# Kernel tuning notes

Hardware: AMD Instinct MI355X
Metric: run time of the kernel (lower is better)

The kernel has to match this reference:

```python
import jax, jax.numpy as jnp
import numpy as np
from jax import lax

EPS = 1e-5
HEADS = 4
NPOINT = 512


def _layernorm(x, g, b):
    mu = jnp.mean(x, axis=-1, keepdims=True)
    var = jnp.var(x, axis=-1, keepdims=True)
    return (x - mu) * lax.rsqrt(var + EPS) * g + b


def farthest_point_sample(xyz, npoint):
    # xyz: [B, N, 3] -> idx [B, npoint]  (canonical PointNet++ FPS, seeded at point 0)
    B, N, _ = xyz.shape

    def step(carry, _):
        dist, far = carry  # [B,N], [B]
        centroid = jnp.take_along_axis(xyz, far[:, None, None], axis=1)  # [B,1,3]
        d = jnp.sum((xyz - centroid) ** 2, axis=-1)  # [B,N]
        dist = jnp.minimum(dist, d)
        nxt = jnp.argmax(dist, axis=1).astype(jnp.int32)
        return (dist, nxt), far

    init = (jnp.full((B, N), 1e10, xyz.dtype), jnp.zeros((B,), jnp.int32))
    _, idx = lax.scan(step, init, None, length=npoint)  # [npoint, B]
    return idx.T  # [B, npoint]


def index_points(points, idx):
    # points: [B, N, D], idx: [B, S] -> [B, S, D]
    return jnp.take_along_axis(points, idx[..., None], axis=1)


def setup_inputs() -> dict:
    key = jax.random.key(0)
    ks = iter(jax.random.split(key, 16))
    B, N, Cin, D, Dff, Dout = 8, 2048, 64, 128, 512, 256
    w = lambda k, s: (jax.random.normal(k, s, jnp.float32) * 0.02)
    inp = {
        "xyz": jax.random.normal(next(ks), (B, 3, N), jnp.float32),
        "points": jax.random.normal(next(ks), (B, Cin, N), jnp.float32),
        "W_proj": w(next(ks), (D, Cin)), "b_proj": jnp.zeros((D,)),
        "bn1_g": jnp.ones((D,)), "bn1_b": jnp.zeros((D,)),
        "bn1_m": jnp.zeros((D,)), "bn1_v": jnp.ones((D,)),
        "W_pos": w(next(ks), (D, 3)), "b_pos": jnp.zeros((D,)),
        "Wq": w(next(ks), (D, D)), "bq": jnp.zeros((D,)),
        "Wk": w(next(ks), (D, D)), "bk": jnp.zeros((D,)),
        "Wv": w(next(ks), (D, D)), "bv": jnp.zeros((D,)),
        "Wo": w(next(ks), (D, D)), "bo": jnp.zeros((D,)),
        "ln1_g": jnp.ones((D,)), "ln1_b": jnp.zeros((D,)),
        "W1": w(next(ks), (Dff, D)), "b1": jnp.zeros((Dff,)),
        "W2": w(next(ks), (D, Dff)), "b2": jnp.zeros((D,)),
        "ln2_g": jnp.ones((D,)), "ln2_b": jnp.zeros((D,)),
        "W_fc": w(next(ks), (Dout, D + 3)), "b_fc": jnp.zeros((Dout,)),
        "bn2_g": jnp.ones((Dout,)), "bn2_b": jnp.zeros((Dout,)),
        "bn2_m": jnp.zeros((Dout,)), "bn2_v": jnp.ones((Dout,)),
    }
    return inp


def reference(xyz, points, W_proj, b_proj, bn1_g, bn1_b, bn1_m, bn1_v,
              W_pos, b_pos, Wq, bq, Wk, bk, Wv, bv, Wo, bo,
              ln1_g, ln1_b, W1, b1, W2, b2, ln2_g, ln2_b,
              W_fc, b_fc, bn2_g, bn2_b, bn2_m, bn2_v):
    B, _, N = xyz.shape
    D = W_proj.shape[0]
    hd = D // HEADS

    # project: pointwise conv + BN (inference), output [B, N, D]
    feat = jnp.einsum('dc,bcn->bnd', W_proj, points) + b_proj
    feat = (feat - bn1_m) * lax.rsqrt(bn1_v + EPS) * bn1_g + bn1_b

    # transformer block with xyz positional encoding
    pos = jnp.einsum('dc,bcn->bnd', W_pos, xyz) + b_pos
    x = feat + pos
    q = (x @ Wq.T + bq).reshape(B, N, HEADS, hd)
    k = (x @ Wk.T + bk).reshape(B, N, HEADS, hd)
    v = (x @ Wv.T + bv).reshape(B, N, HEADS, hd)
    scores = jnp.einsum('bnhd,bmhd->bhnm', q, k) / jnp.sqrt(jnp.float32(hd))
    attn = jax.nn.softmax(scores, axis=-1)
    o = jnp.einsum('bhnm,bmhd->bnhd', attn, v).reshape(B, N, D)
    x = _layernorm(x + (o @ Wo.T + bo), ln1_g, ln1_b)
    ffn = jax.nn.relu(x @ W1.T + b1) @ W2.T + b2
    features = _layernorm(x + ffn, ln2_g, ln2_b)  # [B, N, D]

    # sampling + gather
    xyz_t = jnp.transpose(xyz, (0, 2, 1))  # [B, N, 3]
    fps_idx = farthest_point_sample(xyz_t, NPOINT)  # [B, npoint]
    new_points = index_points(features, fps_idx)    # [B, npoint, D]
    new_xyz = index_points(xyz_t, fps_idx)          # [B, npoint, 3]

    cat = jnp.concatenate([new_points, new_xyz], axis=-1)  # [B, npoint, D+3]
    out = jnp.einsum('od,bnd->bon', W_fc, cat) + b_fc[None, :, None]
    out = (out - bn2_m[None, :, None]) * lax.rsqrt(bn2_v + EPS)[None, :, None] \
          * bn2_g[None, :, None] + bn2_b[None, :, None]
    out = jax.nn.relu(out)  # [B, Dout, npoint]

    return jnp.transpose(new_xyz, (0, 2, 1)), out
```

## Files before the change

### kernel.cpp

```cpp
#include <hip/hip_runtime.h>
#include <hip/hip_bf16.h>

#define B_    8
#define N_    2048
#define CIN_  64
#define D_    128
#define DFF_  512
#define DOUT_ 256
#define S_    512
#define H_    4
#define HD_   32
#define EPS_  1e-5f

typedef unsigned short u16;
typedef unsigned long long u64;
typedef __attribute__((ext_vector_type(8))) short short8v;
typedef __attribute__((ext_vector_type(4))) float f32x4;

__device__ __forceinline__ u16 f2bu(float f) {
  __hip_bfloat16 h = __float2bfloat16(f);
  return *(u16*)&h;
}
__device__ __forceinline__ float bu2f(u16 u) {
  __hip_bfloat16 h = *(__hip_bfloat16*)&u;
  return __bfloat162float(h);
}

#define OW_QKV 0
#define OW_O   49152
#define OW_1   65536
#define OW_2   131072
#define OW_FC  196608
#define OW_CAT 237568
#define NW_TOT 249856

__global__ __launch_bounds__(256) void prep_kernel(
    const float* __restrict__ Wq, const float* __restrict__ bq,
    const float* __restrict__ Wk, const float* __restrict__ bk,
    const float* __restrict__ Wv, const float* __restrict__ bv,
    const float* __restrict__ Wo, const float* __restrict__ W1,
    const float* __restrict__ W2, const float* __restrict__ Wfc,
    const float* __restrict__ bfc, const float* __restrict__ Wp,
    const float* __restrict__ bp, const float* __restrict__ Wpos,
    const float* __restrict__ bpos, const float* __restrict__ g1,
    const float* __restrict__ be1, const float* __restrict__ m1,
    const float* __restrict__ v1, const float* __restrict__ g2,
    const float* __restrict__ bb2, const float* __restrict__ m2,
    const float* __restrict__ v2, u16* __restrict__ wb,
    float* __restrict__ fb) {
  const float SC = 0.1767766952966369f;
  int i = blockIdx.x * 256 + threadIdx.x;
  if (i < OW_O) {
    int n = i >> 7, k = i & 127;
    float v = (n < 128) ? Wq[i] * SC
                        : (n < 256) ? Wk[(n - 128) * 128 + k]
                                    : Wv[(n - 256) * 128 + k];
    wb[OW_QKV + i] = f2bu(v);
  } else if (i < OW_1) {
    wb[i] = f2bu(Wo[i - OW_O]);
  } else if (i < OW_2) {
    wb[i] = f2bu(W1[i - OW_1]);
  } else if (i < OW_FC) {
    wb[i] = f2bu(W2[i - OW_2]);
  } else if (i < OW_CAT) {
    int j = i - OW_FC;
    int n = j / 160, c = j % 160;
    wb[i] = f2bu(c < 131 ? Wfc[n * 131 + c] : 0.f);
  } else if (i < NW_TOT) {
    int j = i - OW_CAT;
    int d = j / 96, c = j % 96;
    float v;
    if (c < 64) v = Wp[d * 64 + c] * (g1[d] * rsqrtf(v1[d] + EPS_));
    else if (c < 67) v = Wpos[d * 3 + (c - 64)];
    else v = 0.f;
    wb[i] = f2bu(v);
  } else if (i < NW_TOT + 384) {
    int n = i - NW_TOT;
    fb[n] = (n < 128) ? bq[n] * SC : (n < 256) ? bk[n - 128] : bv[n - 256];
  } else if (i < NW_TOT + 512) {
    int d = i - (NW_TOT + 384);
    float s1 = g1[d] * rsqrtf(v1[d] + EPS_);
    fb[384 + d] = (bp[d] - m1[d]) * s1 + be1[d] + bpos[d];
  } else if (i < NW_TOT + 768) {
    int n = i - (NW_TOT + 512);
    fb[512 + n] = g2[n] * rsqrtf(v2[n] + EPS_);
  } else if (i < NW_TOT + 1024) {
    int n = i - (NW_TOT + 768);
    float s = g2[n] * rsqrtf(v2[n] + EPS_);
    fb[768 + n] = bfc[n] * s + bb2[n] - m2[n] * s;
  }
}

#define FPS_SMEM 256

template <int CTRL, int RM>
__device__ __forceinline__ float dppmax(float v) {
  int m = __builtin_amdgcn_update_dpp(__float_as_int(v), __float_as_int(v),
                                      CTRL, RM, 0xF, true);
  return fmaxf(v, __int_as_float(m));
}

__device__ __forceinline__ void fps_slice(
    char* smem, int b, const float* __restrict__ xyz,
    float* __restrict__ dist_ws, int* __restrict__ far_ws,
    int* __restrict__ idx_out, float* __restrict__ out0, int s0, int s1) {
  u64* keys = (u64*)smem;
  float* crd = (float*)(smem + 64);
  const int t = threadIdx.x, w = t >> 6, lane = t & 63;
  const float* xb = xyz + (size_t)b * 3 * N_;
  const int base = w * 512 + lane * 8;
  float* dw = dist_ws + b * N_;
  float px[8], py[8], pz[8], dist[8];
#pragma unroll
  for (int j = 0; j < 8; j++) {
    px[j] = xb[base + j];
    py[j] = xb[N_ + base + j];
    pz[j] = xb[2 * N_ + base + j];
    dist[j] = 1e10f;
  }
  if (s0 != 0) {
#pragma unroll
    for (int j = 0; j < 8; j++) dist[j] = dw[base + j];
  }
  int far = (s0 == 0) ? 0 : far_ws[b];
  float cx = xb[far], cy = xb[N_ + far], cz = xb[2 * N_ + far];
  for (int s = s0; s < s1; s++) {
    if (t == 0) {
      idx_out[b * S_ + s] = far;
      out0[(size_t)b * 3 * S_ + s] = cx;
      out0[(size_t)b * 3 * S_ + S_ + s] = cy;
      out0[(size_t)b * 3 * S_ + 2 * S_ + s] = cz;
    }
    float best = -1.0f, bx = 0.f, by = 0.f, bz = 0.f;
    int bestp = 0;
#pragma unroll
    for (int j = 0; j < 8; j++) {
      float dx = __fsub_rn(px[j], cx);
      float dy = __fsub_rn(py[j], cy);
      float dz = __fsub_rn(pz[j], cz);
      float d = __fadd_rn(__fadd_rn(__fmul_rn(dx, dx), __fmul_rn(dy, dy)),
                          __fmul_rn(dz, dz));
      float nd = fminf(dist[j], d);
      dist[j] = nd;
      if (nd > best) {
        best = nd; bestp = base + j;
        bx = px[j]; by = py[j]; bz = pz[j];
      }
    }
    float m = best;
    m = dppmax<0x111, 0xF>(m);
    m = dppmax<0x112, 0xF>(m);
    m = dppmax<0x114, 0xF>(m);
    m = dppmax<0x118, 0xF>(m);
    m = dppmax<0x142, 0xA>(m);
    m = dppmax<0x143, 0xC>(m);
    float M = __int_as_float(__builtin_amdgcn_readlane(__float_as_int(m), 63));
    u64 mask = __ballot(best == M);
    int wl = __ffsll((long long)mask) - 1;
    if (lane == wl) {
      int sb = (s & 1) * 4 + w;
      keys[sb] = ((u64)__float_as_uint(M) << 32) |
                 (unsigned)(0xFFFFFFFFu - (unsigned)bestp);
      crd[sb * 3 + 0] = bx;
      crd[sb * 3 + 1] = by;
      crd[sb * 3 + 2] = bz;
    }
    asm volatile("s_waitcnt lgkmcnt(0)" ::: "memory");
    __builtin_amdgcn_s_barrier();
    asm volatile("" ::: "memory");
    const int q0 = (s & 1) * 4;
    u64 k0 = keys[q0], k1 = keys[q0 + 1], k2 = keys[q0 + 2], k3 = keys[q0 + 3];
    float x0 = crd[q0 * 3 + 0], y0 = crd[q0 * 3 + 1], z0 = crd[q0 * 3 + 2];
    float x1 = crd[q0 * 3 + 3], y1 = crd[q0 * 3 + 4], z1 = crd[q0 * 3 + 5];
    float x2 = crd[q0 * 3 + 6], y2 = crd[q0 * 3 + 7], z2 = crd[q0 * 3 + 8];
    float x3 = crd[q0 * 3 + 9], y3 = crd[q0 * 3 + 10], z3 = crd[q0 * 3 + 11];
    bool c01 = k0 >= k1;
    u64 ka = c01 ? k0 : k1;
    float xa = c01 ? x0 : x1, ya = c01 ? y0 : y1, za = c01 ? z0 : z1;
    bool c23 = k2 >= k3;
    u64 kb = c23 ? k2 : k3;
    float xv = c23 ? x2 : x3, yv = c23 ? y2 : y3, zv = c23 ? z2 : z3;
    bool cf = ka >= kb;
    u64 kk = cf ? ka : kb;
    cx = cf ? xa : xv; cy = cf ? ya : yv; cz = cf ? za : zv;
    far = (int)(0xFFFFFFFFu - (unsigned)kk);
  }
#pragma unroll
  for (int j = 0; j < 8; j++) dw[base + j] = dist[j];
  if (t == 0) far_ws[b] = far;
}

template <int K, int KC, int ASTAGE, int EPI>
__global__ __launch_bounds__(256) void gemm_k(
    const u16* __restrict__ A, const u16* __restrict__ W,
    const float* __restrict__ srcf0, const float* __restrict__ srcf1,
    const int* __restrict__ fidx, const float* __restrict__ p0,
    const float* __restrict__ p1, const float* __restrict__ p2,
    const u16* __restrict__ resid, u16* __restrict__ outb,
    float* __restrict__ outf, int ntn, int fpsnb, int s0, int s1,
    const float* fxyz, float* fdist, int* ffar, int* fidxo, float* fout0) {
  constexpr int KP = KC + 8;
  constexpr int GEMM_SMEM = 2 * 128 * KP * 2;
  constexpr int SMEM = GEMM_SMEM > FPS_SMEM ? GEMM_SMEM : FPS_SMEM;
  __shared__ __align__(16) char smem[SMEM];
  if ((int)blockIdx.x < fpsnb) {
    fps_slice(smem, blockIdx.x, fxyz, fdist, ffar, fidxo, fout0, s0, s1);
    return;
  }
  u16 (*As)[KP] = (u16 (*)[KP])smem;
  u16 (*Ws)[KP] = (u16 (*)[KP])(smem + 128 * KP * 2);
  const int bid = blockIdx.x - fpsnb;
  const int mt = bid / ntn, nt = bid % ntn;
  const int t = threadIdx.x, w = t >> 6, lane = t & 63;
  const int g = lane >> 4, lr = lane & 15;

  f32x4 acc[2][8];
#pragma unroll
  for (int qf = 0; qf < 2; qf++)
#pragma unroll
    for (int nf = 0; nf < 8; nf++) acc[qf][nf] = {0.f, 0.f, 0.f, 0.f};

  for (int kc = 0; kc < K / KC; kc++) {
    __syncthreads();
    for (int i = t; i < 128 * (KC / 8); i += 256) {
      int row = i / (KC / 8), c8 = i % (KC / 8);
      *(short8v*)&Ws[row][c8 * 8] =
          *(const short8v*)(W + (size_t)(nt * 128 + row) * K + kc * KC + c8 * 8);
    }
    if constexpr (ASTAGE == 0) {
      for (int i = t; i < 128 * (KC / 8); i += 256) {
        int row = i / (KC / 8), c8 = i % (KC / 8);
        *(short8v*)&As[row][c8 * 8] =
            *(const short8v*)(A + (size_t)(mt * 128 + row) * K + kc * KC + c8 * 8);
      }
    } else if constexpr (ASTAGE == 1) {
      int bb = (mt * 128) >> 11, n0 = (mt * 128) & (N_ - 1);
      for (int i = t; i < 96 * 128; i += 256) {
        int c = i >> 7, n = i & 127;
        float v;
        if (c < 64) v = srcf0[((size_t)bb * CIN_ + c) * N_ + n0 + n];
        else if (c < 67) v = srcf1[((size_t)bb * 3 + (c - 64)) * N_ + n0 + n];
        else v = 0.f;
        As[n][c] = f2bu(v);
      }
    } else {
      int bb = (mt * 128) >> 9, sq0 = (mt * 128) & (S_ - 1);
      for (int i = t; i < 128 * 20; i += 256) {
        int row = i / 20, c8 = i % 20;
        int id = fidx[bb * S_ + sq0 + row];
        short8v val;
        if (c8 < 16) {
          val = *(const short8v*)(A + ((size_t)bb * N_ + id) * D_ + c8 * 8);
        } else if (c8 == 16) {
          val = short8v{0, 0, 0, 0, 0, 0, 0, 0};
          val[0] = (short)f2bu(srcf1[((size_t)bb * 3 + 0) * N_ + id]);
          val[1] = (short)f2bu(srcf1[((size_t)bb * 3 + 1) * N_ + id]);
          val[2] = (short)f2bu(srcf1[((size_t)bb * 3 + 2) * N_ + id]);
        } else {
          val = short8v{0, 0, 0, 0, 0, 0, 0, 0};
        }
        *(short8v*)&As[row][c8 * 8] = val;
      }
    }
    __syncthreads();
#pragma unroll
    for (int ks = 0; ks < KC / 32; ks++) {
      short8v a0 = *(const short8v*)&As[w * 32 + lr][ks * 32 + 8 * g];
      short8v a1 = *(const short8v*)&As[w * 32 + 16 + lr][ks * 32 + 8 * g];
#pragma unroll
      for (int nf = 0; nf < 8; nf++) {
        short8v bb = *(const short8v*)&Ws[nf * 16 + lr][ks * 32 + 8 * g];
        acc[0][nf] = __builtin_amdgcn_mfma_f32_16x16x32_bf16(a0, bb, acc[0][nf], 0, 0, 0);
        acc[1][nf] = __builtin_amdgcn_mfma_f32_16x16x32_bf16(a1, bb, acc[1][nf], 0, 0, 0);
      }
    }
  }

  if constexpr (EPI == 3) {
#pragma unroll
    for (int qf = 0; qf < 2; qf++) {
#pragma unroll
      for (int i = 0; i < 4; i++) {
        int m = mt * 128 + w * 32 + qf * 16 + 4 * g + i;
        float v[8], sm = 0.f, sq = 0.f;
#pragma unroll
        for (int nf = 0; nf < 8; nf++) {
          int n = nf * 16 + lr;
          float x = acc[qf][nf][i] + p0[n] + bu2f(resid[(size_t)m * D_ + n]);
          v[nf] = x;
          sm += x;
          sq += x * x;
        }
#pragma unroll
        for (int msk = 1; msk < 16; msk <<= 1) {
          sm += __shfl_xor(sm, msk);
          sq += __shfl_xor(sq, msk);
        }
        float mu = sm * (1.f / 128.f);
        float var = sq * (1.f / 128.f) - mu * mu;
        float rs = rsqrtf(var + EPS_);
#pragma unroll
        for (int nf = 0; nf < 8; nf++) {
          int n = nf * 16 + lr;
          outb[(size_t)m * D_ + n] = f2bu((v[nf] - mu) * rs * p1[n] + p2[n]);
        }
      }
    }
  } else {
#pragma unroll
    for (int qf = 0; qf < 2; qf++)
#pragma unroll
      for (int nf = 0; nf < 8; nf++)
#pragma unroll
        for (int i = 0; i < 4; i++) {
          int m = mt * 128 + w * 32 + qf * 16 + 4 * g + i;
          int nl = nf * 16 + lr;
          int n = nt * 128 + nl;
          float vv = acc[qf][nf][i];
          if constexpr (EPI == 0) {
            outb[(size_t)m * D_ + nl] = f2bu(vv + p0[n]);
          } else if constexpr (EPI == 1) {
            vv += p0[n];
            int which = n >> 7, h = (n >> 5) & 3, c = n & 31;
            int bb = m >> 11, tok = m & (N_ - 1);
            outb[(size_t)which * 2097152 +
                 (((size_t)bb * H_ + h) * N_ + tok) * HD_ + c] = f2bu(vv);
          } else if constexpr (EPI == 2) {
            outb[(size_t)m * DFF_ + n] = f2bu(fmaxf(vv + p0[n], 0.f));
          } else {
            float r = fmaxf(vv * p1[n] + p2[n], 0.f);
            outf[((size_t)(m >> 9) * DOUT_ + n) * S_ + (m & (S_ - 1))] = r;
          }
        }
  }
}

__global__ __launch_bounds__(256) void attn_mfma_kernel(
    const u16* __restrict__ qg, const u16* __restrict__ kg,
    const u16* __restrict__ vg, u16* __restrict__ o, int fpsnb, int s0, int s1,
    const float* fxyz, float* fdist, int* ffar, int* fidxo, float* fout0) {
  constexpr int ATTN_SMEM = 64 * 40 * 2 + 32 * 72 * 2 + 4 * 16 * 72 * 2;
  constexpr int SMEM = ATTN_SMEM > FPS_SMEM ? ATTN_SMEM : FPS_SMEM;
  __shared__ __align__(16) char smem[SMEM];
  if ((int)blockIdx.x < fpsnb) {
    fps_slice(smem, blockIdx.x, fxyz, fdist, ffar, fidxo, fout0, s0, s1);
    return;
  }
  const int t = threadIdx.x;
  const int w = t >> 6, lane = t & 63, g = lane >> 4, lr = lane & 15;
  u16 (*ks)[40] = (u16 (*)[40])smem;
  u16 (*vt)[72] = (u16 (*)[72])(smem + 5120);
  u16 (*psw)[72] = (u16 (*)[72])(smem + 9728) + w * 16;

  const int bid = blockIdx.x - fpsnb;
  const int qt = bid & 31;
  const int bh = bid >> 5;
  const int b = bh >> 2, h = bh & 3;
  const int qrow = qt * 64 + w * 16 + lr;

  short8v aq = *(const short8v*)(qg + ((size_t)bh * N_ + qrow) * HD_ + 8 * g);

  const u16* kb = kg + (size_t)bh * N_ * HD_;
  const u16* vb = vg + (size_t)bh * N_ * HD_;

  const f32x4 fzero = {0.f, 0.f, 0.f, 0.f};
  float mrun = -INFINITY, lrun = 0.f;
  f32x4 acco[2] = {fzero, fzero};

  const int srow = t >> 2, scol = (t & 3) * 8;

  for (int ch = 0; ch < 32; ch++) {
    __syncthreads();
    short8v kvv = *(const short8v*)(kb + (size_t)(ch * 64 + srow) * HD_ + scol);
    short8v vvv = *(const short8v*)(vb + (size_t)(ch * 64 + srow) * HD_ + scol);
    *(short8v*)(&ks[srow][scol]) = kvv;
#pragma unroll
    for (int e = 0; e < 8; e++) vt[scol + e][srow] = (u16)vvv[e];
    __syncthreads();

    f32x4 st[4];
#pragma unroll
    for (int kt = 0; kt < 4; kt++) {
      short8v ak = *(const short8v*)(&ks[kt * 16 + lr][8 * g]);
      st[kt] = __builtin_amdgcn_mfma_f32_16x16x32_bf16(ak, aq, fzero, 0, 0, 0);
    }

    float mx = -INFINITY;
#pragma unroll
    for (int kt = 0; kt < 4; kt++)
#pragma unroll
      for (int i = 0; i < 4; i++) mx = fmaxf(mx, st[kt][i]);
    mx = fmaxf(mx, __shfl_xor(mx, 16));
    mx = fmaxf(mx, __shfl_xor(mx, 32));
    float nm = fmaxf(mrun, mx);
    float alpha = __expf(mrun - nm);
    mrun = nm;
    float psum = 0.f;
#pragma unroll
    for (int kt = 0; kt < 4; kt++) {
      float p0 = __expf(st[kt][0] - nm);
      float p1 = __expf(st[kt][1] - nm);
      float p2 = __expf(st[kt][2] - nm);
      float p3 = __expf(st[kt][3] - nm);
      psum += (p0 + p1) + (p2 + p3);
      u64 pk = (u64)f2bu(p0) | ((u64)f2bu(p1) << 16) |
               ((u64)f2bu(p2) << 32) | ((u64)f2bu(p3) << 48);
      *(u64*)(&psw[lr][kt * 16 + 4 * g]) = pk;
    }
    psum += __shfl_xor(psum, 16);
    psum += __shfl_xor(psum, 32);
    lrun = lrun * alpha + psum;
#pragma unroll
    for (int dt = 0; dt < 2; dt++)
#pragma unroll
      for (int i = 0; i < 4; i++) acco[dt][i] *= alpha;

#pragma unroll
    for (int mc = 0; mc < 2; mc++) {
      short8v pb = *(const short8v*)(&psw[lr][mc * 32 + 8 * g]);
#pragma unroll
      for (int dt = 0; dt < 2; dt++) {
        short8v av = *(const short8v*)(&vt[dt * 16 + lr][mc * 32 + 8 * g]);
        acco[dt] = __builtin_amdgcn_mfma_f32_16x16x32_bf16(av, pb, acco[dt], 0, 0, 0);
      }
    }
  }

  float rl = 1.0f / lrun;
#pragma unroll
  for (int dt = 0; dt < 2; dt++) {
    u64 pk = (u64)f2bu(acco[dt][0] * rl) | ((u64)f2bu(acco[dt][1] * rl) << 16) |
             ((u64)f2bu(acco[dt][2] * rl) << 32) |
             ((u64)f2bu(acco[dt][3] * rl) << 48);
    *(u64*)(o + ((size_t)b * N_ + qrow) * D_ + h * HD_ + dt * 16 + 4 * g) = pk;
  }
}

extern "C" void kernel_launch(void* const* d_in, const int* in_sizes, int n_in,
                              void* d_out, int out_size, void* d_ws, size_t ws_size,
                              hipStream_t stream) {
  const float* xyz    = (const float*)d_in[0];
  const float* points = (const float*)d_in[1];
  const float* Wp     = (const float*)d_in[2];
  const float* bp     = (const float*)d_in[3];
  const float* g1     = (const float*)d_in[4];
  const float* be1    = (const float*)d_in[5];
  const float* m1     = (const float*)d_in[6];
  const float* v1     = (const float*)d_in[7];
  const float* Wpos   = (const float*)d_in[8];
  const float* bpos   = (const float*)d_in[9];
  const float* Wq     = (const float*)d_in[10];
  const float* bq     = (const float*)d_in[11];
  const float* Wk     = (const float*)d_in[12];
  const float* bk     = (const float*)d_in[13];
  const float* Wv     = (const float*)d_in[14];
  const float* bv     = (const float*)d_in[15];
  const float* Wo     = (const float*)d_in[16];
  const float* bo     = (const float*)d_in[17];
  const float* lg1    = (const float*)d_in[18];
  const float* lb1    = (const float*)d_in[19];
  const float* W1     = (const float*)d_in[20];
  const float* b1     = (const float*)d_in[21];
  const float* W2     = (const float*)d_in[22];
  const float* b2p    = (const float*)d_in[23];
  const float* lg2    = (const float*)d_in[24];
  const float* lb2    = (const float*)d_in[25];
  const float* Wfc    = (const float*)d_in[26];
  const float* bfc    = (const float*)d_in[27];
  const float* g2     = (const float*)d_in[28];
  const float* bb2    = (const float*)d_in[29];
  const float* m2     = (const float*)d_in[30];
  const float* v2     = (const float*)d_in[31];

  float* out0 = (float*)d_out;
  float* out1 = out0 + (size_t)B_ * 3 * S_;

  char* ws = (char*)d_ws;
  int*   fps_idx = (int*)ws;
  u16*   wb      = (u16*)(ws + 16384);
  float* fb      = (float*)(ws + 516096);
  float* dist_ws = (float*)(ws + 520192);
  int*   far_ws  = (int*)(ws + 585728);
  const size_t MB = 1024 * 1024;
  u16* x     = (u16*)(ws + 1 * MB);
  u16* o     = (u16*)(ws + 5 * MB);
  u16* x2    = (u16*)(ws + 9 * MB);
  u16* feats = (u16*)(ws + 13 * MB);
  u16* qb    = (u16*)(ws + 17 * MB);
  u16* h     = (u16*)(ws + 29 * MB);

  prep_kernel<<<980, 256, 0, stream>>>(Wq, bq, Wk, bk, Wv, bv, Wo, W1, W2, Wfc,
                                       bfc, Wp, bp, Wpos, bpos, g1, be1, m1, v1,
                                       g2, bb2, m2, v2, wb, fb);

  gemm_k<96, 96, 1, 0><<<8 + 128, 256, 0, stream>>>(
      nullptr, wb + OW_CAT, points, xyz, nullptr, fb + 384, nullptr, nullptr,
      nullptr, x, nullptr, 1, 8, 0, 70, xyz, dist_ws, far_ws, fps_idx, out0);
  gemm_k<128, 128, 0, 1><<<8 + 384, 256, 0, stream>>>(
      x, wb + OW_QKV, nullptr, nullptr, nullptr, fb, nullptr, nullptr,
      nullptr, qb, nullptr, 3, 8, 70, 160, xyz, dist_ws, far_ws, fps_idx, out0);
  attn_mfma_kernel<<<8 + B_ * H_ * (N_ / 64), 256, 0, stream>>>(
      qb, qb + 2097152, qb + 2 * 2097152, o, 8, 160, 260, xyz, dist_ws, far_ws,
      fps_idx, out0);
  gemm_k<128, 128, 0, 3><<<8 + 128, 256, 0, stream>>>(
      o, wb + OW_O, nullptr, nullptr, nullptr, bo, lg1, lb1, x, x2, nullptr, 1,
      8, 260, 330, xyz, dist_ws, far_ws, fps_idx, out0);
  gemm_k<128, 128, 0, 2><<<8 + 512, 256, 0, stream>>>(
      x2, wb + OW_1, nullptr, nullptr, nullptr, b1, nullptr, nullptr,
      nullptr, h, nullptr, 4, 8, 330, 440, xyz, dist_ws, far_ws, fps_idx, out0);
  gemm_k<512, 128, 0, 3><<<8 + 128, 256, 0, stream>>>(
      h, wb + OW_2, nullptr, nullptr, nullptr, b2p, lg2, lb2, x2, feats,
      nullptr, 1, 8, 440, 512, xyz, dist_ws, far_ws, fps_idx, out0);
  gemm_k<160, 160, 2, 4><<<64, 256, 0, stream>>>(
      feats, wb + OW_FC, nullptr, xyz, fps_idx, nullptr, fb + 512, fb + 768,
      nullptr, nullptr, out1, 2, 0, 0, 0, nullptr, nullptr, nullptr, nullptr,
      nullptr);
}
```

Measured before the change: 360.6 us.

## Widen attention blocks to 512 threads, swizzle LDS, rebalance FPS slices

The attention kernel moves to 512-thread blocks covering 128 query rows, with K and V staging split between the two thread halves. The transposed V and P tiles get XOR-style swizzled LDS layouts to avoid bank conflicts. The softmax now uses exp2 with log2(e) folded into the Q scale. FPS is templated on the wave count so the co-scheduled FPS blocks in attention run 8 waves with 4 points per lane at raised priority, and the FPS step ranges per kernel are shifted to give attention a larger share. The aim is to shorten the serial FPS critical path hidden behind the GEMMs and to speed up attention, at the cost of more LDS per block and possibly lower occupancy.

```diff
diff --git a/kernel.cpp b/kernel.cpp
--- a/kernel.cpp
+++ b/kernel.cpp
@@ -48,7 +48,7 @@
     const float* __restrict__ bb2, const float* __restrict__ m2,
     const float* __restrict__ v2, u16* __restrict__ wb,
     float* __restrict__ fb) {
-  const float SC = 0.1767766952966369f;
+  const float SC = 0.1767766952966369f * 1.4426950408889634f;
   int i = blockIdx.x * 256 + threadIdx.x;
   if (i < OW_O) {
     int n = i >> 7, k = i & 127;
@@ -91,7 +91,7 @@
   }
 }
 
-#define FPS_SMEM 256
+#define FPS_SMEM 320
 
 template <int CTRL, int RM>
 __device__ __forceinline__ float dppmax(float v) {
@@ -100,19 +100,22 @@
   return fmaxf(v, __int_as_float(m));
 }
 
+template <int NW>
 __device__ __forceinline__ void fps_slice(
     char* smem, int b, const float* __restrict__ xyz,
     float* __restrict__ dist_ws, int* __restrict__ far_ws,
     int* __restrict__ idx_out, float* __restrict__ out0, int s0, int s1) {
+  constexpr int PPL = 2048 / (NW * 64);
   u64* keys = (u64*)smem;
-  float* crd = (float*)(smem + 64);
+  float* crd = (float*)(smem + 2 * NW * 8);
+  __builtin_amdgcn_s_setprio(3);
   const int t = threadIdx.x, w = t >> 6, lane = t & 63;
   const float* xb = xyz + (size_t)b * 3 * N_;
-  const int base = w * 512 + lane * 8;
+  const int base = (w * 64 + lane) * PPL;
   float* dw = dist_ws + b * N_;
-  float px[8], py[8], pz[8], dist[8];
-#pragma unroll
-  for (int j = 0; j < 8; j++) {
+  float px[PPL], py[PPL], pz[PPL], dist[PPL];
+#pragma unroll
+  for (int j = 0; j < PPL; j++) {
     px[j] = xb[base + j];
     py[j] = xb[N_ + base + j];
     pz[j] = xb[2 * N_ + base + j];
@@ -120,7 +123,7 @@
   }
   if (s0 != 0) {
 #pragma unroll
-    for (int j = 0; j < 8; j++) dist[j] = dw[base + j];
+    for (int j = 0; j < PPL; j++) dist[j] = dw[base + j];
   }
   int far = (s0 == 0) ? 0 : far_ws[b];
   float cx = xb[far], cy = xb[N_ + far], cz = xb[2 * N_ + far];
@@ -134,7 +137,7 @@
     float best = -1.0f, bx = 0.f, by = 0.f, bz = 0.f;
     int bestp = 0;
 #pragma unroll
-    for (int j = 0; j < 8; j++) {
+    for (int j = 0; j < PPL; j++) {
       float dx = __fsub_rn(px[j], cx);
       float dy = __fsub_rn(py[j], cy);
       float dz = __fsub_rn(pz[j], cz);
@@ -158,7 +161,7 @@
     u64 mask = __ballot(best == M);
     int wl = __ffsll((long long)mask) - 1;
     if (lane == wl) {
-      int sb = (s & 1) * 4 + w;
+      int sb = (s & 1) * NW + w;
       keys[sb] = ((u64)__float_as_uint(M) << 32) |
                  (unsigned)(0xFFFFFFFFu - (unsigned)bestp);
       crd[sb * 3 + 0] = bx;
@@ -168,26 +171,25 @@
     asm volatile("s_waitcnt lgkmcnt(0)" ::: "memory");
     __builtin_amdgcn_s_barrier();
     asm volatile("" ::: "memory");
-    const int q0 = (s & 1) * 4;
-    u64 k0 = keys[q0], k1 = keys[q0 + 1], k2 = keys[q0 + 2], k3 = keys[q0 + 3];
-    float x0 = crd[q0 * 3 + 0], y0 = crd[q0 * 3 + 1], z0 = crd[q0 * 3 + 2];
-    float x1 = crd[q0 * 3 + 3], y1 = crd[q0 * 3 + 4], z1 = crd[q0 * 3 + 5];
-    float x2 = crd[q0 * 3 + 6], y2 = crd[q0 * 3 + 7], z2 = crd[q0 * 3 + 8];
-    float x3 = crd[q0 * 3 + 9], y3 = crd[q0 * 3 + 10], z3 = crd[q0 * 3 + 11];
-    bool c01 = k0 >= k1;
-    u64 ka = c01 ? k0 : k1;
-    float xa = c01 ? x0 : x1, ya = c01 ? y0 : y1, za = c01 ? z0 : z1;
-    bool c23 = k2 >= k3;
-    u64 kb = c23 ? k2 : k3;
-    float xv = c23 ? x2 : x3, yv = c23 ? y2 : y3, zv = c23 ? z2 : z3;
-    bool cf = ka >= kb;
-    u64 kk = cf ? ka : kb;
-    cx = cf ? xa : xv; cy = cf ? ya : yv; cz = cf ? za : zv;
+    const int q0 = (s & 1) * NW;
+    u64 kk = keys[q0];
+    float ccx = crd[q0 * 3], ccy = crd[q0 * 3 + 1], ccz = crd[q0 * 3 + 2];
+#pragma unroll
+    for (int i = 1; i < NW; i++) {
+      u64 ki = keys[q0 + i];
+      bool c = ki > kk;
+      kk = c ? ki : kk;
+      ccx = c ? crd[(q0 + i) * 3] : ccx;
+      ccy = c ? crd[(q0 + i) * 3 + 1] : ccy;
+      ccz = c ? crd[(q0 + i) * 3 + 2] : ccz;
+    }
     far = (int)(0xFFFFFFFFu - (unsigned)kk);
-  }
-#pragma unroll
-  for (int j = 0; j < 8; j++) dw[base + j] = dist[j];
+    cx = ccx; cy = ccy; cz = ccz;
+  }
+#pragma unroll
+  for (int j = 0; j < PPL; j++) dw[base + j] = dist[j];
   if (t == 0) far_ws[b] = far;
+  __builtin_amdgcn_s_setprio(0);
 }
 
 template <int K, int KC, int ASTAGE, int EPI>
@@ -204,7 +206,7 @@
   constexpr int SMEM = GEMM_SMEM > FPS_SMEM ? GEMM_SMEM : FPS_SMEM;
   __shared__ __align__(16) char smem[SMEM];
   if ((int)blockIdx.x < fpsnb) {
-    fps_slice(smem, blockIdx.x, fxyz, fdist, ffar, fidxo, fout0, s0, s1);
+    fps_slice<4>(smem, blockIdx.x, fxyz, fdist, ffar, fidxo, fout0, s0, s1);
     return;
   }
   u16 (*As)[KP] = (u16 (*)[KP])smem;
@@ -335,28 +337,28 @@
   }
 }
 
-__global__ __launch_bounds__(256) void attn_mfma_kernel(
+__global__ __launch_bounds__(512) void attn_mfma_kernel(
     const u16* __restrict__ qg, const u16* __restrict__ kg,
     const u16* __restrict__ vg, u16* __restrict__ o, int fpsnb, int s0, int s1,
     const float* fxyz, float* fdist, int* ffar, int* fidxo, float* fout0) {
-  constexpr int ATTN_SMEM = 64 * 40 * 2 + 32 * 72 * 2 + 4 * 16 * 72 * 2;
+  constexpr int ATTN_SMEM = 5120 + 4096 + 8 * 2048;
   constexpr int SMEM = ATTN_SMEM > FPS_SMEM ? ATTN_SMEM : FPS_SMEM;
   __shared__ __align__(16) char smem[SMEM];
   if ((int)blockIdx.x < fpsnb) {
-    fps_slice(smem, blockIdx.x, fxyz, fdist, ffar, fidxo, fout0, s0, s1);
+    fps_slice<8>(smem, blockIdx.x, fxyz, fdist, ffar, fidxo, fout0, s0, s1);
     return;
   }
   const int t = threadIdx.x;
   const int w = t >> 6, lane = t & 63, g = lane >> 4, lr = lane & 15;
   u16 (*ks)[40] = (u16 (*)[40])smem;
-  u16 (*vt)[72] = (u16 (*)[72])(smem + 5120);
-  u16 (*psw)[72] = (u16 (*)[72])(smem + 9728) + w * 16;
+  u16* vtb = (u16*)(smem + 5120);
+  u16* pswb = (u16*)(smem + 9216) + w * 1024;
 
   const int bid = blockIdx.x - fpsnb;
-  const int qt = bid & 31;
-  const int bh = bid >> 5;
+  const int qt = bid & 15;
+  const int bh = bid >> 4;
   const int b = bh >> 2, h = bh & 3;
-  const int qrow = qt * 64 + w * 16 + lr;
+  const int qrow = qt * 128 + w * 16 + lr;
 
   short8v aq = *(const short8v*)(qg + ((size_t)bh * N_ + qrow) * HD_ + 8 * g);
 
@@ -367,45 +369,54 @@
   float mrun = -INFINITY, lrun = 0.f;
   f32x4 acco[2] = {fzero, fzero};
 
-  const int srow = t >> 2, scol = (t & 3) * 8;
+  const int st_ = t & 255;
+  const int srow = st_ >> 2, scol = (st_ & 3) * 8;
 
   for (int ch = 0; ch < 32; ch++) {
     __syncthreads();
-    short8v kvv = *(const short8v*)(kb + (size_t)(ch * 64 + srow) * HD_ + scol);
-    short8v vvv = *(const short8v*)(vb + (size_t)(ch * 64 + srow) * HD_ + scol);
-    *(short8v*)(&ks[srow][scol]) = kvv;
-#pragma unroll
-    for (int e = 0; e < 8; e++) vt[scol + e][srow] = (u16)vvv[e];
+    if (t < 256) {
+      short8v kvv = *(const short8v*)(kb + (size_t)(ch * 64 + srow) * HD_ + scol);
+      *(short8v*)(&ks[srow][scol]) = kvv;
+    } else {
+      short8v vvv = *(const short8v*)(vb + (size_t)(ch * 64 + srow) * HD_ + scol);
+#pragma unroll
+      for (int e = 0; e < 8; e++) {
+        int d = scol + e;
+        vtb[d * 64 + ((((srow >> 3) + (d >> 3)) & 7) << 3) + (srow & 7)] =
+            (u16)vvv[e];
+      }
+    }
     __syncthreads();
 
-    f32x4 st[4];
+    f32x4 stv[4];
 #pragma unroll
     for (int kt = 0; kt < 4; kt++) {
       short8v ak = *(const short8v*)(&ks[kt * 16 + lr][8 * g]);
-      st[kt] = __builtin_amdgcn_mfma_f32_16x16x32_bf16(ak, aq, fzero, 0, 0, 0);
+      stv[kt] = __builtin_amdgcn_mfma_f32_16x16x32_bf16(ak, aq, fzero, 0, 0, 0);
     }
 
     float mx = -INFINITY;
 #pragma unroll
     for (int kt = 0; kt < 4; kt++)
 #pragma unroll
-      for (int i = 0; i < 4; i++) mx = fmaxf(mx, st[kt][i]);
+      for (int i = 0; i < 4; i++) mx = fmaxf(mx, stv[kt][i]);
     mx = fmaxf(mx, __shfl_xor(mx, 16));
     mx = fmaxf(mx, __shfl_xor(mx, 32));
     float nm = fmaxf(mrun, mx);
-    float alpha = __expf(mrun - nm);
+    float alpha = exp2f(mrun - nm);
     mrun = nm;
     float psum = 0.f;
 #pragma unroll
     for (int kt = 0; kt < 4; kt++) {
-      float p0 = __expf(st[kt][0] - nm);
-      float p1 = __expf(st[kt][1] - nm);
-      float p2 = __expf(st[kt][2] - nm);
-      float p3 = __expf(st[kt][3] - nm);
+      float p0 = exp2f(stv[kt][0] - nm);
+      float p1 = exp2f(stv[kt][1] - nm);
+      float p2 = exp2f(stv[kt][2] - nm);
+      float p3 = exp2f(stv[kt][3] - nm);
       psum += (p0 + p1) + (p2 + p3);
       u64 pk = (u64)f2bu(p0) | ((u64)f2bu(p1) << 16) |
                ((u64)f2bu(p2) << 32) | ((u64)f2bu(p3) << 48);
-      *(u64*)(&psw[lr][kt * 16 + 4 * g]) = pk;
+      int off = lr * 64 + ((((2 * kt + (g >> 1)) + lr) & 7) << 3) + ((g & 1) << 2);
+      *(u64*)(pswb + off) = pk;
     }
     psum += __shfl_xor(psum, 16);
     psum += __shfl_xor(psum, 32);
@@ -417,10 +428,13 @@
 
 #pragma unroll
     for (int mc = 0; mc < 2; mc++) {
-      short8v pb = *(const short8v*)(&psw[lr][mc * 32 + 8 * g]);
+      short8v pb = *(const short8v*)(pswb + lr * 64 +
+                                     ((((mc * 4 + g) + lr) & 7) << 3));
 #pragma unroll
       for (int dt = 0; dt < 2; dt++) {
-        short8v av = *(const short8v*)(&vt[dt * 16 + lr][mc * 32 + 8 * g]);
+        int row = 16 * dt + lr;
+        short8v av = *(const short8v*)(vtb + row * 64 +
+                                       ((((mc * 4 + g) + (row >> 3)) & 7) << 3));
         acco[dt] = __builtin_amdgcn_mfma_f32_16x16x32_bf16(av, pb, acco[dt], 0, 0, 0);
       }
     }
@@ -495,22 +509,22 @@
 
   gemm_k<96, 96, 1, 0><<<8 + 128, 256, 0, stream>>>(
       nullptr, wb + OW_CAT, points, xyz, nullptr, fb + 384, nullptr, nullptr,
-      nullptr, x, nullptr, 1, 8, 0, 70, xyz, dist_ws, far_ws, fps_idx, out0);
+      nullptr, x, nullptr, 1, 8, 0, 48, xyz, dist_ws, far_ws, fps_idx, out0);
   gemm_k<128, 128, 0, 1><<<8 + 384, 256, 0, stream>>>(
       x, wb + OW_QKV, nullptr, nullptr, nullptr, fb, nullptr, nullptr,
-      nullptr, qb, nullptr, 3, 8, 70, 160, xyz, dist_ws, far_ws, fps_idx, out0);
-  attn_mfma_kernel<<<8 + B_ * H_ * (N_ / 64), 256, 0, stream>>>(
-      qb, qb + 2097152, qb + 2 * 2097152, o, 8, 160, 260, xyz, dist_ws, far_ws,
+      nullptr, qb, nullptr, 3, 8, 48, 112, xyz, dist_ws, far_ws, fps_idx, out0);
+  attn_mfma_kernel<<<8 + B_ * H_ * (N_ / 128), 512, 0, stream>>>(
+      qb, qb + 2097152, qb + 2 * 2097152, o, 8, 112, 352, xyz, dist_ws, far_ws,
       fps_idx, out0);
   gemm_k<128, 128, 0, 3><<<8 + 128, 256, 0, stream>>>(
       o, wb + OW_O, nullptr, nullptr, nullptr, bo, lg1, lb1, x, x2, nullptr, 1,
-      8, 260, 330, xyz, dist_ws, far_ws, fps_idx, out0);
+      8, 352, 392, xyz, dist_ws, far_ws, fps_idx, out0);
   gemm_k<128, 128, 0, 2><<<8 + 512, 256, 0, stream>>>(
       x2, wb + OW_1, nullptr, nullptr, nullptr, b1, nullptr, nullptr,
-      nullptr, h, nullptr, 4, 8, 330, 440, xyz, dist_ws, far_ws, fps_idx, out0);
+      nullptr, h, nullptr, 4, 8, 392, 448, xyz, dist_ws, far_ws, fps_idx, out0);
   gemm_k<512, 128, 0, 3><<<8 + 128, 256, 0, stream>>>(
       h, wb + OW_2, nullptr, nullptr, nullptr, b2p, lg2, lb2, x2, feats,
-      nullptr, 1, 8, 440, 512, xyz, dist_ws, far_ws, fps_idx, out0);
+      nullptr, 1, 8, 448, 512, xyz, dist_ws, far_ws, fps_idx, out0);
   gemm_k<160, 160, 2, 4><<<64, 256, 0, stream>>>(
       feats, wb + OW_FC, nullptr, xyz, fps_idx, nullptr, fb + 512, fb + 768,
       nullptr, nullptr, out1, 2, 0, 0, 0, nullptr, nullptr, nullptr, nullptr,
```

Result: slower. 425.3 us (+18.0%).
